# Kernel optimization log

Measured on AMD Instinct MI355X. Metric: run time of the kernel, lower is better.

Reference implementation:

```python
import jax, jax.numpy as jnp
import numpy as np
from math import isqrt

NUM_HEADS = 8
EPS = 1e-12  # torch F.normalize default eps


def _l2_normalize_seq(t):
    # normalize over the sequence axis (dim=-2), matching F.normalize(t, dim=-2)
    n = jnp.sqrt(jnp.sum(t * t, axis=-2, keepdims=True))
    return t / jnp.maximum(n, EPS)


def setup_inputs() -> dict:
    key = jax.random.key(0)
    ks = jax.random.split(key, 7)
    B, L, C = 8, 4096, 384
    s = 0.02
    return {
        "x": jax.random.normal(ks[0], (B, L, C), jnp.float32),
        "qkv_w": jax.random.normal(ks[1], (3 * C, C), jnp.float32) * s,
        "qkv_b": jax.random.normal(ks[2], (3 * C,), jnp.float32) * s,
        "proj_w": jax.random.normal(ks[3], (C, C), jnp.float32) * s,
        "proj_b": jax.random.normal(ks[4], (C,), jnp.float32) * s,
        "temperature": jnp.ones((NUM_HEADS, 1, 1), jnp.float32),
        "conv_w": jax.random.normal(ks[5], (C, 1, 3, 3), jnp.float32) * s,
        "conv_b": jax.random.normal(ks[6], (C,), jnp.float32) * s,
    }


def reference(x, qkv_w, qkv_b, proj_w, proj_b, temperature, conv_w, conv_b):
    B, L, C = x.shape
    h = NUM_HEADS
    d = C // h
    H = W = isqrt(L)

    # qkv projection -> (3, B, h, L, d)
    qkv = (x @ qkv_w.T + qkv_b).reshape(B, L, 3, h, d).transpose(2, 0, 3, 1, 4)
    q, k, v = qkv[0], qkv[1], qkv[2]

    # L2 normalize q, k over sequence axis
    q = _l2_normalize_seq(q)
    k = _l2_normalize_seq(k)

    # LePE: depthwise 3x3 conv on v in image layout (B, C, H, W)
    v_img = v.transpose(0, 1, 3, 2).reshape(B, C, H, W)
    lepe = jax.lax.conv_general_dilated(
        v_img, conv_w, window_strides=(1, 1), padding=((1, 1), (1, 1)),
        feature_group_count=C,
        dimension_numbers=("NCHW", "OIHW", "NCHW"),
    ) + conv_b[None, :, None, None]
    lepe = lepe.reshape(B, h, d, L).transpose(0, 1, 3, 2)  # (B, h, L, d)

    # linear attention: attn = (k^T v) * temperature, shape (B, h, d, d)
    attn = jnp.einsum("bhld,bhle->bhde", k, v) * temperature
    out = jnp.einsum("bhld,bhde->bhle", q, attn) + lepe  # (B, h, L, d)

    out = out.transpose(0, 2, 1, 3).reshape(B, L, C)
    out = out @ proj_w.T + proj_b
    return (out, attn)
```

## Files before the change

### kernel.cpp

```cpp
#include <hip/hip_runtime.h>
#include <hip/hip_bf16.h>


typedef __bf16 bf16x8 __attribute__((ext_vector_type(8)));
typedef float f32x4 __attribute__((ext_vector_type(4)));

__device__ inline __bf16 f2b(float f) {
    __hip_bfloat16 h = __float2bfloat16(f);
    __bf16 r; __builtin_memcpy(&r, &h, 2); return r;
}
__device__ inline float b2f(__hip_bfloat16 h) { return __bfloat162float(h); }
__device__ inline float b2f(__bf16 v) {
    __hip_bfloat16 h; __builtin_memcpy(&h, &v, 2); return __bfloat162float(h);
}

__device__ inline bf16x8 load8(const __hip_bfloat16* p) {
    uint4 v = *(const uint4*)p;
    bf16x8 r; __builtin_memcpy(&r, &v, 16); return r;
}
__device__ inline bf16x8 load8(const float* p) {
    float4 a = *(const float4*)p;
    float4 b = *(const float4*)(p + 4);
    bf16x8 r;
    r[0] = f2b(a.x); r[1] = f2b(a.y); r[2] = f2b(a.z); r[3] = f2b(a.w);
    r[4] = f2b(b.x); r[5] = f2b(b.y); r[6] = f2b(b.z); r[7] = f2b(b.w);
    return r;
}

__device__ inline void storef(float* p, float v) { *p = v; }
__device__ inline void storef(__hip_bfloat16* p, float v) { *p = __float2bfloat16(v); }

__device__ inline void gl_lds16(const __hip_bfloat16* g, __hip_bfloat16* l) {
    __builtin_amdgcn_global_load_lds(
        (const __attribute__((address_space(1))) void*)g,
        (__attribute__((address_space(3))) void*)l,
        16, 0, 0);
}

__global__ __launch_bounds__(256) void cvt_kernel(
    const float* __restrict__ x,  __hip_bfloat16* __restrict__ xb,
    const float* __restrict__ qw, __hip_bfloat16* __restrict__ qwb,
    const float* __restrict__ pw, __hip_bfloat16* __restrict__ pwb)
{
    int blk = blockIdx.x;
    const float* src; __hip_bfloat16* dst; int base;
    if (blk < 6144)      { src = x;  dst = xb;  base = blk; }
    else if (blk < 6360) { src = qw; dst = qwb; base = blk - 6144; }
    else                 { src = pw; dst = pwb; base = blk - 6360; }
    int i = base * 256 + threadIdx.x;
    bf16x8 v = load8(src + (size_t)i * 8);
    *(bf16x8*)(dst + (size_t)i * 8) = v;
}

template <typename TO, int KC, bool FUSE_SQ>
__global__ __launch_bounds__(256) void gemm_bf16_nt(
    const __hip_bfloat16* __restrict__ A,
    const __hip_bfloat16* __restrict__ Bw,
    const float* __restrict__ bias,
    TO* __restrict__ C,
    int N, int NXT,
    float* __restrict__ sq)
{
    __shared__ __hip_bfloat16 As[128 * 64];
    __shared__ __hip_bfloat16 Bs[64 * 64];
    const int t = threadIdx.x;
    const int w = t >> 6, lane = t & 63;
    const int r16 = lane & 15, quad = lane >> 4;
    const int bx  = blockIdx.x;
    const int xcd = bx & 7, seq = bx >> 3;
    const int n_t = seq % NXT, m_t = seq / NXT;
    const int m0 = (xcd + 8 * m_t) * 128;
    const int n0 = n_t * 64;
    const int wm = w >> 1, wn = w & 1;

    f32x4 acc[4][2];
    #pragma unroll
    for (int mi = 0; mi < 4; ++mi)
        #pragma unroll
        for (int ni = 0; ni < 2; ++ni)
            acc[mi][ni] = (f32x4){0.f, 0.f, 0.f, 0.f};

    for (int k0 = 0; k0 < KC; k0 += 64) {
        #pragma unroll
        for (int p = 0; p < 4; ++p) {
            int c = p * 64 + lane;
            int rl = c >> 3;
            int cc = (c & 7) ^ (rl & 7);
            gl_lds16(A + (size_t)(m0 + w * 32 + rl) * KC + k0 + cc * 8,
                     &As[(w * 256 + c) * 8]);
        }
        #pragma unroll
        for (int p = 0; p < 2; ++p) {
            int c = p * 64 + lane;
            int rl = c >> 3;
            int cc = (c & 7) ^ (rl & 7);
            gl_lds16(Bw + (size_t)(n0 + w * 16 + rl) * KC + k0 + cc * 8,
                     &Bs[(w * 128 + c) * 8]);
        }
        __syncthreads();
        bf16x8 af[4][2], bfr[2][2];
        #pragma unroll
        for (int ks = 0; ks < 2; ++ks) {
            #pragma unroll
            for (int mi = 0; mi < 4; ++mi) {
                int row = wm * 64 + mi * 16 + r16;
                int pc  = (ks * 4 + quad) ^ (r16 & 7);
                af[mi][ks] = *(const bf16x8*)&As[row * 64 + pc * 8];
            }
            #pragma unroll
            for (int ni = 0; ni < 2; ++ni) {
                int row = wn * 32 + ni * 16 + r16;
                int pc  = (ks * 4 + quad) ^ (r16 & 7);
                bfr[ni][ks] = *(const bf16x8*)&Bs[row * 64 + pc * 8];
            }
        }
        #pragma unroll
        for (int ks = 0; ks < 2; ++ks)
            #pragma unroll
            for (int mi = 0; mi < 4; ++mi)
                #pragma unroll
                for (int ni = 0; ni < 2; ++ni)
                    acc[mi][ni] = __builtin_amdgcn_mfma_f32_16x16x32_bf16(
                        af[mi][ks], bfr[ni][ks], acc[mi][ni], 0, 0, 0);
        __syncthreads();
    }

    #pragma unroll
    for (int ni = 0; ni < 2; ++ni) {
        int col = n0 + wn * 32 + ni * 16 + r16;
        float bv = bias[col];
        float s = 0.f;
        #pragma unroll
        for (int mi = 0; mi < 4; ++mi) {
            #pragma unroll
            for (int reg = 0; reg < 4; ++reg) {
                int row = m0 + wm * 64 + mi * 16 + quad * 4 + reg;
                float o = acc[mi][ni][reg] + bv;
                storef(&C[(size_t)row * N + col], o);
                s += o * o;
            }
        }
        if constexpr (FUSE_SQ) {
            if (col < 768) {
                s += __shfl_xor(s, 16);
                s += __shfl_xor(s, 32);
                if (quad == 0) {
                    int b = m0 >> 12;
                    atomicAdd(&sq[b * 768 + col], s);
                }
            }
        }
    }
}

__global__ void invnorm_kernel(const float* __restrict__ sumsq, float* __restrict__ invn)
{
    int i = blockIdx.x * 256 + threadIdx.x;
    if (i < 6144) invn[i] = 1.f / fmaxf(sqrtf(sumsq[i]), 1e-12f);
}

__global__ __launch_bounds__(256) void ktv_mfma_kernel(
    const __hip_bfloat16* __restrict__ qkv, float* __restrict__ G)
{
    __shared__ __hip_bfloat16 kT[4][48][40];
    __shared__ __hip_bfloat16 vT[4][48][40];
    __shared__ float red[4][48][49];

    const int bh = blockIdx.y; const int b = bh >> 3; const int h = bh & 7;
    const int lbase = blockIdx.x * 1024;
    const int t = threadIdx.x;
    const int w = t >> 6, lane = t & 63;
    const int r16 = lane & 15, quad = lane >> 4;

    f32x4 acc[3][3];
    #pragma unroll
    for (int mi = 0; mi < 3; ++mi)
        #pragma unroll
        for (int ni = 0; ni < 3; ++ni)
            acc[mi][ni] = (f32x4){0.f, 0.f, 0.f, 0.f};

    const int mat  = t & 1;
    const int lrow = t >> 1;
    const int tile = lrow >> 5, l_in = lrow & 31;
    const __hip_bfloat16* src = qkv + 384 + mat * 384 + h * 48;
    __hip_bfloat16* dstT = (mat ? &vT[0][0][0] : &kT[0][0][0]) + ((size_t)tile * 48 * 40 + l_in);

    for (int it = 0; it < 8; ++it) {
        const int l0 = lbase + it * 128;
        const __hip_bfloat16* p = src + (size_t)(b * 4096 + l0 + lrow) * 1152;
        __hip_bfloat16 row[48];
        #pragma unroll
        for (int j = 0; j < 6; ++j) {
            uint4 v = *(const uint4*)(p + j * 8);
            __builtin_memcpy(&row[j * 8], &v, 16);
        }
        #pragma unroll
        for (int d = 0; d < 48; ++d)
            dstT[d * 40] = row[d];
        __syncthreads();

        bf16x8 af[3], bfr[3];
        #pragma unroll
        for (int mi = 0; mi < 3; ++mi)
            af[mi] = *(const bf16x8*)&kT[w][mi * 16 + r16][quad * 8];
        #pragma unroll
        for (int ni = 0; ni < 3; ++ni)
            bfr[ni] = *(const bf16x8*)&vT[w][ni * 16 + r16][quad * 8];
        #pragma unroll
        for (int mi = 0; mi < 3; ++mi)
            #pragma unroll
            for (int ni = 0; ni < 3; ++ni)
                acc[mi][ni] = __builtin_amdgcn_mfma_f32_16x16x32_bf16(af[mi], bfr[ni], acc[mi][ni], 0, 0, 0);
        __syncthreads();
    }

    #pragma unroll
    for (int mi = 0; mi < 3; ++mi)
        #pragma unroll
        for (int ni = 0; ni < 3; ++ni)
            #pragma unroll
            for (int reg = 0; reg < 4; ++reg)
                red[w][mi * 16 + quad * 4 + reg][ni * 16 + r16] = acc[mi][ni][reg];
    __syncthreads();

    float* Gb = G + (size_t)bh * 2304;
    for (int cell = t; cell < 2304; cell += 256) {
        int row = cell / 48, col = cell % 48;
        float s = red[0][row][col] + red[1][row][col] + red[2][row][col] + red[3][row][col];
        atomicAdd(&Gb[cell], s);
    }
}

__global__ void scale_attn_kernel(
    const float* __restrict__ G, const float* __restrict__ invn,
    const float* __restrict__ temp,
    float* __restrict__ attn_out, float* __restrict__ attn2)
{
    int bh = blockIdx.x; int b = bh >> 3; int h = bh & 7;
    float tf = temp[h];
    int t = threadIdx.x;
    for (int e = t; e < 2304; e += 256) {
        int dk = e / 48;
        float ink = invn[b * 768 + 384 + h * 48 + dk];
        float inq = invn[b * 768 + h * 48 + dk];
        float av  = G[(size_t)bh * 2304 + e] * ink * tf;
        attn_out[(size_t)bh * 2304 + e] = av;
        attn2[(size_t)bh * 2304 + e]    = av * inq;
    }
}

__global__ __launch_bounds__(256) void qattn_lepe_mfma(
    const __hip_bfloat16* __restrict__ qkv, const float* __restrict__ attn2,
    const float* __restrict__ conv_w, const float* __restrict__ conv_b,
    __hip_bfloat16* __restrict__ y)
{
    __shared__ __attribute__((aligned(16))) char smem[26624];
    __hip_bfloat16 (*qs)[72]  = (__hip_bfloat16 (*)[72])smem;
    __hip_bfloat16 (*a2s)[72] = (__hip_bfloat16 (*)[72])(smem + 18432);
    float (*ys)[52]           = (float (*)[52])smem;
    __shared__ __hip_bfloat16 vs[4][64][48];
    __shared__ float cwT[9][48];
    __shared__ float cb[48];

    const int bh = blockIdx.y; const int b = bh >> 3; const int h = bh & 7;
    const int yi0 = blockIdx.x * 2;
    const int l0  = yi0 * 64;
    const int t = threadIdx.x;
    const int w = t >> 6, lane = t & 63;
    const int r16 = lane & 15, quad = lane >> 4;

    const __hip_bfloat16* qbase = qkv + (size_t)(b * 4096 + l0) * 1152 + h * 48;
    #pragma unroll
    for (int i = 0; i < 3; ++i) {
        int chunk = t + i * 256;
        int row = chunk / 6, cg = chunk % 6;
        *(bf16x8*)&qs[row][cg * 8] = load8(qbase + (size_t)row * 1152 + cg * 8);
    }
    *(bf16x8*)&qs[t >> 1][48 + (t & 1) * 8] = (bf16x8)0;

    const float* a2g = attn2 + (size_t)bh * 2304;
    for (int i = t; i < 3072; i += 256) {
        int e = i >> 6, dd = i & 63;
        float val = (dd < 48) ? a2g[dd * 48 + e] : 0.f;
        a2s[e][dd] = __float2bfloat16(val);
    }

    const __hip_bfloat16* vbase = qkv + (size_t)b * 4096 * 1152 + 768 + h * 48;
    #pragma unroll
    for (int i = 0; i < 6; ++i) {
        int chunk = t + i * 256;
        int r = chunk / 384, rem = chunk % 384;
        int xx = rem / 6, cg = rem % 6;
        int yy = yi0 - 1 + r;
        bf16x8 v = (yy >= 0 && yy < 64)
            ? load8(vbase + (size_t)(yy * 64 + xx) * 1152 + cg * 8)
            : (bf16x8)0;
        *(bf16x8*)&vs[r][xx][cg * 8] = v;
    }

    for (int i = t; i < 432; i += 256)
        cwT[i / 48][i % 48] = conv_w[(h * 48 + (i % 48)) * 9 + (i / 48)];
    if (t < 48) cb[t] = conv_b[h * 48 + t];
    __syncthreads();

    f32x4 acc[2][3];
    #pragma unroll
    for (int mi = 0; mi < 2; ++mi)
        #pragma unroll
        for (int ni = 0; ni < 3; ++ni)
            acc[mi][ni] = (f32x4){0.f, 0.f, 0.f, 0.f};
    #pragma unroll
    for (int ks = 0; ks < 2; ++ks) {
        int kb = ks * 32 + quad * 8;
        bf16x8 af[2], bfr[3];
        #pragma unroll
        for (int mi = 0; mi < 2; ++mi)
            af[mi] = *(const bf16x8*)&qs[w * 32 + mi * 16 + r16][kb];
        #pragma unroll
        for (int ni = 0; ni < 3; ++ni)
            bfr[ni] = *(const bf16x8*)&a2s[ni * 16 + r16][kb];
        #pragma unroll
        for (int mi = 0; mi < 2; ++mi)
            #pragma unroll
            for (int ni = 0; ni < 3; ++ni)
                acc[mi][ni] = __builtin_amdgcn_mfma_f32_16x16x32_bf16(af[mi], bfr[ni], acc[mi][ni], 0, 0, 0);
    }
    __syncthreads();

    #pragma unroll
    for (int mi = 0; mi < 2; ++mi)
        #pragma unroll
        for (int ni = 0; ni < 3; ++ni)
            #pragma unroll
            for (int reg = 0; reg < 4; ++reg)
                ys[w * 32 + mi * 16 + quad * 4 + reg][ni * 16 + r16] = acc[mi][ni][reg];
    __syncthreads();

    __hip_bfloat16* ybase = y + (size_t)(b * 4096 + l0) * 384 + h * 48;
    #pragma unroll
    for (int i = 0; i < 3; ++i) {
        int g = t + i * 256;
        int l_in = g / 6, cg = g % 6, e0 = cg * 8;
        int xi = l_in & 63, vr0 = l_in >> 6;
        float o[8];
        #pragma unroll
        for (int j = 0; j < 8; ++j) o[j] = ys[l_in][e0 + j] + cb[e0 + j];
        #pragma unroll
        for (int dy = 0; dy < 3; ++dy) {
            #pragma unroll
            for (int dx = 0; dx < 3; ++dx) {
                int xx = xi + dx - 1;
                if (xx < 0 || xx > 63) continue;
                bf16x8 vv = *(const bf16x8*)&vs[vr0 + dy][xx][e0];
                const float* cwp = &cwT[dy * 3 + dx][e0];
                #pragma unroll
                for (int j = 0; j < 8; ++j) o[j] += b2f(vv[j]) * cwp[j];
            }
        }
        __hip_bfloat16 ob[8];
        #pragma unroll
        for (int j = 0; j < 8; ++j) ob[j] = __float2bfloat16(o[j]);
        uint4 pk; __builtin_memcpy(&pk, ob, 16);
        *(uint4*)(ybase + (size_t)l_in * 384 + e0) = pk;
    }
}

extern "C" void kernel_launch(void* const* d_in, const int* in_sizes, int n_in,
                              void* d_out, int out_size, void* d_ws, size_t ws_size,
                              hipStream_t stream)
{
    const float* x      = (const float*)d_in[0];
    const float* qkv_w  = (const float*)d_in[1];
    const float* qkv_b  = (const float*)d_in[2];
    const float* proj_w = (const float*)d_in[3];
    const float* proj_b = (const float*)d_in[4];
    const float* temp   = (const float*)d_in[5];
    const float* conv_w = (const float*)d_in[6];
    const float* conv_b = (const float*)d_in[7];

    char* ws = (char*)d_ws;
    __hip_bfloat16* qkv = (__hip_bfloat16*)(ws);
    __hip_bfloat16* yb  = (__hip_bfloat16*)(ws + 75497472);
    float* sumsq = (float*)(ws + 100663296);
    float* G     = (float*)(ws + 100687872);
    float* invn  = (float*)(ws + 101277696);
    float* attn2 = (float*)(ws + 101302272);
    __hip_bfloat16* x_bf16  = yb;
    __hip_bfloat16* qkv_wb  = (__hip_bfloat16*)(ws + 101892096);
    __hip_bfloat16* proj_wb = (__hip_bfloat16*)(ws + 102776832);

    float* out      = (float*)d_out;
    float* attn_out = out + 12582912;

    (void)hipMemsetAsync(ws + 100663296, 0, 614400, stream);

    cvt_kernel<<<6432, 256, 0, stream>>>(x, x_bf16, qkv_w, qkv_wb, proj_w, proj_wb);
    gemm_bf16_nt<__hip_bfloat16, 384, true><<<4608, 256, 0, stream>>>(
        x_bf16, qkv_wb, qkv_b, qkv, 1152, 18, sumsq);
    invnorm_kernel<<<24, 256, 0, stream>>>(sumsq, invn);
    ktv_mfma_kernel<<<dim3(4, 64), 256, 0, stream>>>(qkv, G);
    scale_attn_kernel<<<64, 256, 0, stream>>>(G, invn, temp, attn_out, attn2);
    qattn_lepe_mfma<<<dim3(32, 64), 256, 0, stream>>>(qkv, attn2, conv_w, conv_b, yb);
    gemm_bf16_nt<float, 384, false><<<1536, 256, 0, stream>>>(
        yb, proj_wb, proj_b, out, 384, 6, nullptr);
}
```

Before: 226.1 us.

## Fuse x fp32-to-bf16 conversion into QKV GEMM and drop invnorm kernel

The QKV GEMM now reads fp32 x directly and converts it to bf16 in registers before storing to LDS, so the separate conversion pass that wrote and re-read a bf16 copy of x goes away. The inverse-norm computation moves into scale_attn_kernel through shared memory, which removes one launch. The k^T v kernel is split across 4x more blocks (256 rows each instead of 1024) to raise occupancy, at the cost of more atomic adds into G. The A-tile load in the QKV GEMM loses its asynchronous global-to-LDS path and now takes twice the bytes through registers.

```diff
diff --git a/kernel.cpp b/kernel.cpp
--- a/kernel.cpp
+++ b/kernel.cpp
@@ -38,23 +38,21 @@
 }
 
 __global__ __launch_bounds__(256) void cvt_kernel(
-    const float* __restrict__ x,  __hip_bfloat16* __restrict__ xb,
     const float* __restrict__ qw, __hip_bfloat16* __restrict__ qwb,
     const float* __restrict__ pw, __hip_bfloat16* __restrict__ pwb)
 {
     int blk = blockIdx.x;
     const float* src; __hip_bfloat16* dst; int base;
-    if (blk < 6144)      { src = x;  dst = xb;  base = blk; }
-    else if (blk < 6360) { src = qw; dst = qwb; base = blk - 6144; }
-    else                 { src = pw; dst = pwb; base = blk - 6360; }
+    if (blk < 216) { src = qw; dst = qwb; base = blk; }
+    else           { src = pw; dst = pwb; base = blk - 216; }
     int i = base * 256 + threadIdx.x;
     bf16x8 v = load8(src + (size_t)i * 8);
     *(bf16x8*)(dst + (size_t)i * 8) = v;
 }
 
-template <typename TO, int KC, bool FUSE_SQ>
+template <typename TA, typename TO, int KC, bool FUSE_SQ>
 __global__ __launch_bounds__(256) void gemm_bf16_nt(
-    const __hip_bfloat16* __restrict__ A,
+    const TA* __restrict__ A,
     const __hip_bfloat16* __restrict__ Bw,
     const float* __restrict__ bias,
     TO* __restrict__ C,
@@ -82,20 +80,36 @@
 
     for (int k0 = 0; k0 < KC; k0 += 64) {
         #pragma unroll
-        for (int p = 0; p < 4; ++p) {
-            int c = p * 64 + lane;
-            int rl = c >> 3;
-            int cc = (c & 7) ^ (rl & 7);
-            gl_lds16(A + (size_t)(m0 + w * 32 + rl) * KC + k0 + cc * 8,
-                     &As[(w * 256 + c) * 8]);
-        }
-        #pragma unroll
         for (int p = 0; p < 2; ++p) {
             int c = p * 64 + lane;
             int rl = c >> 3;
             int cc = (c & 7) ^ (rl & 7);
             gl_lds16(Bw + (size_t)(n0 + w * 16 + rl) * KC + k0 + cc * 8,
                      &Bs[(w * 128 + c) * 8]);
+        }
+        if constexpr (__is_same(TA, float)) {
+            #pragma unroll
+            for (int p = 0; p < 4; ++p) {
+                int c = p * 64 + lane;
+                int rl = c >> 3;
+                int cc = (c & 7) ^ (rl & 7);
+                const float* src = A + (size_t)(m0 + w * 32 + rl) * KC + k0 + cc * 8;
+                float4 a = *(const float4*)src;
+                float4 b = *(const float4*)(src + 4);
+                bf16x8 r;
+                r[0] = f2b(a.x); r[1] = f2b(a.y); r[2] = f2b(a.z); r[3] = f2b(a.w);
+                r[4] = f2b(b.x); r[5] = f2b(b.y); r[6] = f2b(b.z); r[7] = f2b(b.w);
+                *(bf16x8*)&As[(w * 256 + c) * 8] = r;
+            }
+        } else {
+            #pragma unroll
+            for (int p = 0; p < 4; ++p) {
+                int c = p * 64 + lane;
+                int rl = c >> 3;
+                int cc = (c & 7) ^ (rl & 7);
+                gl_lds16(A + (size_t)(m0 + w * 32 + rl) * KC + k0 + cc * 8,
+                         &As[(w * 256 + c) * 8]);
+            }
         }
         __syncthreads();
         bf16x8 af[4][2], bfr[2][2];
@@ -153,12 +167,6 @@
     }
 }
 
-__global__ void invnorm_kernel(const float* __restrict__ sumsq, float* __restrict__ invn)
-{
-    int i = blockIdx.x * 256 + threadIdx.x;
-    if (i < 6144) invn[i] = 1.f / fmaxf(sqrtf(sumsq[i]), 1e-12f);
-}
-
 __global__ __launch_bounds__(256) void ktv_mfma_kernel(
     const __hip_bfloat16* __restrict__ qkv, float* __restrict__ G)
 {
@@ -167,7 +175,7 @@
     __shared__ float red[4][48][49];
 
     const int bh = blockIdx.y; const int b = bh >> 3; const int h = bh & 7;
-    const int lbase = blockIdx.x * 1024;
+    const int lbase = blockIdx.x * 256;
     const int t = threadIdx.x;
     const int w = t >> 6, lane = t & 63;
     const int r16 = lane & 15, quad = lane >> 4;
@@ -185,7 +193,7 @@
     const __hip_bfloat16* src = qkv + 384 + mat * 384 + h * 48;
     __hip_bfloat16* dstT = (mat ? &vT[0][0][0] : &kT[0][0][0]) + ((size_t)tile * 48 * 40 + l_in);
 
-    for (int it = 0; it < 8; ++it) {
+    for (int it = 0; it < 2; ++it) {
         const int l0 = lbase + it * 128;
         const __hip_bfloat16* p = src + (size_t)(b * 4096 + l0 + lrow) * 1152;
         __hip_bfloat16 row[48];
@@ -232,20 +240,24 @@
 }
 
 __global__ void scale_attn_kernel(
-    const float* __restrict__ G, const float* __restrict__ invn,
+    const float* __restrict__ G, const float* __restrict__ sumsq,
     const float* __restrict__ temp,
     float* __restrict__ attn_out, float* __restrict__ attn2)
 {
     int bh = blockIdx.x; int b = bh >> 3; int h = bh & 7;
     float tf = temp[h];
     int t = threadIdx.x;
+    __shared__ float ink_s[48], inq_s[48];
+    if (t < 48) {
+        ink_s[t] = 1.f / fmaxf(sqrtf(sumsq[b * 768 + 384 + h * 48 + t]), 1e-12f);
+        inq_s[t] = 1.f / fmaxf(sqrtf(sumsq[b * 768 +       h * 48 + t]), 1e-12f);
+    }
+    __syncthreads();
     for (int e = t; e < 2304; e += 256) {
         int dk = e / 48;
-        float ink = invn[b * 768 + 384 + h * 48 + dk];
-        float inq = invn[b * 768 + h * 48 + dk];
-        float av  = G[(size_t)bh * 2304 + e] * ink * tf;
+        float av  = G[(size_t)bh * 2304 + e] * ink_s[dk] * tf;
         attn_out[(size_t)bh * 2304 + e] = av;
-        attn2[(size_t)bh * 2304 + e]    = av * inq;
+        attn2[(size_t)bh * 2304 + e]    = av * inq_s[dk];
     }
 }
 
@@ -383,9 +395,7 @@
     __hip_bfloat16* yb  = (__hip_bfloat16*)(ws + 75497472);
     float* sumsq = (float*)(ws + 100663296);
     float* G     = (float*)(ws + 100687872);
-    float* invn  = (float*)(ws + 101277696);
     float* attn2 = (float*)(ws + 101302272);
-    __hip_bfloat16* x_bf16  = yb;
     __hip_bfloat16* qkv_wb  = (__hip_bfloat16*)(ws + 101892096);
     __hip_bfloat16* proj_wb = (__hip_bfloat16*)(ws + 102776832);
 
@@ -394,13 +404,12 @@
 
     (void)hipMemsetAsync(ws + 100663296, 0, 614400, stream);
 
-    cvt_kernel<<<6432, 256, 0, stream>>>(x, x_bf16, qkv_w, qkv_wb, proj_w, proj_wb);
-    gemm_bf16_nt<__hip_bfloat16, 384, true><<<4608, 256, 0, stream>>>(
-        x_bf16, qkv_wb, qkv_b, qkv, 1152, 18, sumsq);
-    invnorm_kernel<<<24, 256, 0, stream>>>(sumsq, invn);
-    ktv_mfma_kernel<<<dim3(4, 64), 256, 0, stream>>>(qkv, G);
-    scale_attn_kernel<<<64, 256, 0, stream>>>(G, invn, temp, attn_out, attn2);
+    cvt_kernel<<<288, 256, 0, stream>>>(qkv_w, qkv_wb, proj_w, proj_wb);
+    gemm_bf16_nt<float, __hip_bfloat16, 384, true><<<4608, 256, 0, stream>>>(
+        x, qkv_wb, qkv_b, qkv, 1152, 18, sumsq);
+    ktv_mfma_kernel<<<dim3(16, 64), 256, 0, stream>>>(qkv, G);
+    scale_attn_kernel<<<64, 256, 0, stream>>>(G, sumsq, temp, attn_out, attn2);
     qattn_lepe_mfma<<<dim3(32, 64), 256, 0, stream>>>(qkv, attn2, conv_w, conv_b, yb);
-    gemm_bf16_nt<float, 384, false><<<1536, 256, 0, stream>>>(
+    gemm_bf16_nt<__hip_bfloat16, float, 384, false><<<1536, 256, 0, stream>>>(
         yb, proj_wb, proj_b, out, 384, 6, nullptr);
 }
```

Result: slower. 245.4 us (+8.5%).

## Double-buffer GEMM LDS tiles, fold invnorm into scale kernel, widen k^T v grid

Applied to the files above, without the earlier changes.

The bf16 GEMM now uses two LDS buffers and issues the next K-tile's global-to-LDS loads before the MFMA work on the current tile, to overlap memory with compute. The separate inverse-norm kernel is removed; scale_attn computes the inverse norms itself into shared memory, saving a launch. The k^T v kernel uses four times more blocks, each covering fewer rows, for more parallelism at the cost of more atomic adds. LDS use in the GEMM doubles, which may reduce occupancy.

```diff
diff --git a/kernel.cpp b/kernel.cpp
--- a/kernel.cpp
+++ b/kernel.cpp
@@ -61,8 +61,8 @@
     int N, int NXT,
     float* __restrict__ sq)
 {
-    __shared__ __hip_bfloat16 As[128 * 64];
-    __shared__ __hip_bfloat16 Bs[64 * 64];
+    __shared__ __hip_bfloat16 As[2][128 * 64];
+    __shared__ __hip_bfloat16 Bs[2][64 * 64];
     const int t = threadIdx.x;
     const int w = t >> 6, lane = t & 63;
     const int r16 = lane & 15, quad = lane >> 4;
@@ -80,14 +80,14 @@
         for (int ni = 0; ni < 2; ++ni)
             acc[mi][ni] = (f32x4){0.f, 0.f, 0.f, 0.f};
 
-    for (int k0 = 0; k0 < KC; k0 += 64) {
+    auto stage = [&](int buf, int k0) {
         #pragma unroll
         for (int p = 0; p < 4; ++p) {
             int c = p * 64 + lane;
             int rl = c >> 3;
             int cc = (c & 7) ^ (rl & 7);
             gl_lds16(A + (size_t)(m0 + w * 32 + rl) * KC + k0 + cc * 8,
-                     &As[(w * 256 + c) * 8]);
+                     &As[buf][(w * 256 + c) * 8]);
         }
         #pragma unroll
         for (int p = 0; p < 2; ++p) {
@@ -95,9 +95,17 @@
             int rl = c >> 3;
             int cc = (c & 7) ^ (rl & 7);
             gl_lds16(Bw + (size_t)(n0 + w * 16 + rl) * KC + k0 + cc * 8,
-                     &Bs[(w * 128 + c) * 8]);
-        }
-        __syncthreads();
+                     &Bs[buf][(w * 128 + c) * 8]);
+        }
+    };
+
+    constexpr int NT = KC / 64;
+    stage(0, 0);
+    __syncthreads();
+
+    #pragma unroll
+    for (int ti = 0; ti < NT; ++ti) {
+        const int cur = ti & 1;
         bf16x8 af[4][2], bfr[2][2];
         #pragma unroll
         for (int ks = 0; ks < 2; ++ks) {
@@ -105,15 +113,16 @@
             for (int mi = 0; mi < 4; ++mi) {
                 int row = wm * 64 + mi * 16 + r16;
                 int pc  = (ks * 4 + quad) ^ (r16 & 7);
-                af[mi][ks] = *(const bf16x8*)&As[row * 64 + pc * 8];
+                af[mi][ks] = *(const bf16x8*)&As[cur][row * 64 + pc * 8];
             }
             #pragma unroll
             for (int ni = 0; ni < 2; ++ni) {
                 int row = wn * 32 + ni * 16 + r16;
                 int pc  = (ks * 4 + quad) ^ (r16 & 7);
-                bfr[ni][ks] = *(const bf16x8*)&Bs[row * 64 + pc * 8];
+                bfr[ni][ks] = *(const bf16x8*)&Bs[cur][row * 64 + pc * 8];
             }
         }
+        if (ti + 1 < NT) stage(cur ^ 1, (ti + 1) * 64);
         #pragma unroll
         for (int ks = 0; ks < 2; ++ks)
             #pragma unroll
@@ -153,12 +162,6 @@
     }
 }
 
-__global__ void invnorm_kernel(const float* __restrict__ sumsq, float* __restrict__ invn)
-{
-    int i = blockIdx.x * 256 + threadIdx.x;
-    if (i < 6144) invn[i] = 1.f / fmaxf(sqrtf(sumsq[i]), 1e-12f);
-}
-
 __global__ __launch_bounds__(256) void ktv_mfma_kernel(
     const __hip_bfloat16* __restrict__ qkv, float* __restrict__ G)
 {
@@ -167,7 +170,7 @@
     __shared__ float red[4][48][49];
 
     const int bh = blockIdx.y; const int b = bh >> 3; const int h = bh & 7;
-    const int lbase = blockIdx.x * 1024;
+    const int lbase = blockIdx.x * 256;
     const int t = threadIdx.x;
     const int w = t >> 6, lane = t & 63;
     const int r16 = lane & 15, quad = lane >> 4;
@@ -185,7 +188,7 @@
     const __hip_bfloat16* src = qkv + 384 + mat * 384 + h * 48;
     __hip_bfloat16* dstT = (mat ? &vT[0][0][0] : &kT[0][0][0]) + ((size_t)tile * 48 * 40 + l_in);
 
-    for (int it = 0; it < 8; ++it) {
+    for (int it = 0; it < 2; ++it) {
         const int l0 = lbase + it * 128;
         const __hip_bfloat16* p = src + (size_t)(b * 4096 + l0 + lrow) * 1152;
         __hip_bfloat16 row[48];
@@ -232,20 +235,24 @@
 }
 
 __global__ void scale_attn_kernel(
-    const float* __restrict__ G, const float* __restrict__ invn,
+    const float* __restrict__ G, const float* __restrict__ sumsq,
     const float* __restrict__ temp,
     float* __restrict__ attn_out, float* __restrict__ attn2)
 {
     int bh = blockIdx.x; int b = bh >> 3; int h = bh & 7;
     float tf = temp[h];
     int t = threadIdx.x;
+    __shared__ float ink_s[48], inq_s[48];
+    if (t < 48) {
+        ink_s[t] = 1.f / fmaxf(sqrtf(sumsq[b * 768 + 384 + h * 48 + t]), 1e-12f);
+        inq_s[t] = 1.f / fmaxf(sqrtf(sumsq[b * 768 +       h * 48 + t]), 1e-12f);
+    }
+    __syncthreads();
     for (int e = t; e < 2304; e += 256) {
         int dk = e / 48;
-        float ink = invn[b * 768 + 384 + h * 48 + dk];
-        float inq = invn[b * 768 + h * 48 + dk];
-        float av  = G[(size_t)bh * 2304 + e] * ink * tf;
+        float av  = G[(size_t)bh * 2304 + e] * ink_s[dk] * tf;
         attn_out[(size_t)bh * 2304 + e] = av;
-        attn2[(size_t)bh * 2304 + e]    = av * inq;
+        attn2[(size_t)bh * 2304 + e]    = av * inq_s[dk];
     }
 }
 
@@ -383,7 +390,6 @@
     __hip_bfloat16* yb  = (__hip_bfloat16*)(ws + 75497472);
     float* sumsq = (float*)(ws + 100663296);
     float* G     = (float*)(ws + 100687872);
-    float* invn  = (float*)(ws + 101277696);
     float* attn2 = (float*)(ws + 101302272);
     __hip_bfloat16* x_bf16  = yb;
     __hip_bfloat16* qkv_wb  = (__hip_bfloat16*)(ws + 101892096);
@@ -397,9 +403,8 @@
     cvt_kernel<<<6432, 256, 0, stream>>>(x, x_bf16, qkv_w, qkv_wb, proj_w, proj_wb);
     gemm_bf16_nt<__hip_bfloat16, 384, true><<<4608, 256, 0, stream>>>(
         x_bf16, qkv_wb, qkv_b, qkv, 1152, 18, sumsq);
-    invnorm_kernel<<<24, 256, 0, stream>>>(sumsq, invn);
-    ktv_mfma_kernel<<<dim3(4, 64), 256, 0, stream>>>(qkv, G);
-    scale_attn_kernel<<<64, 256, 0, stream>>>(G, invn, temp, attn_out, attn2);
+    ktv_mfma_kernel<<<dim3(16, 64), 256, 0, stream>>>(qkv, G);
+    scale_attn_kernel<<<64, 256, 0, stream>>>(G, sumsq, temp, attn_out, attn2);
     qattn_lepe_mfma<<<dim3(32, 64), 256, 0, stream>>>(qkv, attn2, conv_w, conv_b, yb);
     gemm_bf16_nt<float, 384, false><<<1536, 256, 0, stream>>>(
         yb, proj_wb, proj_b, out, 384, 6, nullptr);
```

Measured after the change: 222.8 us. Within noise of the previous version (-1.5%).

## Fold norm and attn scaling into qattn kernel, zero accumulators in cvt, widen ktv grid

Applied to the files above, without the earlier changes.

Removes the invnorm and scale_attn kernels and the memset. The inverse norms and temperature scaling are now computed inside qattn_lepe_mfma from sumsq and the raw G, and block x==0 writes attn_out. Zeroing of the accumulators moves into extra blocks of cvt_kernel. ktv is split into 16 blocks per head instead of 4 to raise parallelism, at the cost of more atomic adds on G and redundant per-block norm computation.

```diff
diff --git a/kernel.cpp b/kernel.cpp
--- a/kernel.cpp
+++ b/kernel.cpp
@@ -40,9 +40,14 @@
 __global__ __launch_bounds__(256) void cvt_kernel(
     const float* __restrict__ x,  __hip_bfloat16* __restrict__ xb,
     const float* __restrict__ qw, __hip_bfloat16* __restrict__ qwb,
-    const float* __restrict__ pw, __hip_bfloat16* __restrict__ pwb)
+    const float* __restrict__ pw, __hip_bfloat16* __restrict__ pwb,
+    uint4* __restrict__ zdst)
 {
     int blk = blockIdx.x;
+    if (blk >= 6432) {
+        zdst[(size_t)(blk - 6432) * 256 + threadIdx.x] = (uint4){0, 0, 0, 0};
+        return;
+    }
     const float* src; __hip_bfloat16* dst; int base;
     if (blk < 6144)      { src = x;  dst = xb;  base = blk; }
     else if (blk < 6360) { src = qw; dst = qwb; base = blk - 6144; }
@@ -153,12 +158,6 @@
     }
 }
 
-__global__ void invnorm_kernel(const float* __restrict__ sumsq, float* __restrict__ invn)
-{
-    int i = blockIdx.x * 256 + threadIdx.x;
-    if (i < 6144) invn[i] = 1.f / fmaxf(sqrtf(sumsq[i]), 1e-12f);
-}
-
 __global__ __launch_bounds__(256) void ktv_mfma_kernel(
     const __hip_bfloat16* __restrict__ qkv, float* __restrict__ G)
 {
@@ -167,7 +166,7 @@
     __shared__ float red[4][48][49];
 
     const int bh = blockIdx.y; const int b = bh >> 3; const int h = bh & 7;
-    const int lbase = blockIdx.x * 1024;
+    const int lbase = blockIdx.x * 256;
     const int t = threadIdx.x;
     const int w = t >> 6, lane = t & 63;
     const int r16 = lane & 15, quad = lane >> 4;
@@ -185,7 +184,7 @@
     const __hip_bfloat16* src = qkv + 384 + mat * 384 + h * 48;
     __hip_bfloat16* dstT = (mat ? &vT[0][0][0] : &kT[0][0][0]) + ((size_t)tile * 48 * 40 + l_in);
 
-    for (int it = 0; it < 8; ++it) {
+    for (int it = 0; it < 2; ++it) {
         const int l0 = lbase + it * 128;
         const __hip_bfloat16* p = src + (size_t)(b * 4096 + l0 + lrow) * 1152;
         __hip_bfloat16 row[48];
@@ -231,28 +230,11 @@
     }
 }
 
-__global__ void scale_attn_kernel(
-    const float* __restrict__ G, const float* __restrict__ invn,
-    const float* __restrict__ temp,
-    float* __restrict__ attn_out, float* __restrict__ attn2)
-{
-    int bh = blockIdx.x; int b = bh >> 3; int h = bh & 7;
-    float tf = temp[h];
-    int t = threadIdx.x;
-    for (int e = t; e < 2304; e += 256) {
-        int dk = e / 48;
-        float ink = invn[b * 768 + 384 + h * 48 + dk];
-        float inq = invn[b * 768 + h * 48 + dk];
-        float av  = G[(size_t)bh * 2304 + e] * ink * tf;
-        attn_out[(size_t)bh * 2304 + e] = av;
-        attn2[(size_t)bh * 2304 + e]    = av * inq;
-    }
-}
-
 __global__ __launch_bounds__(256) void qattn_lepe_mfma(
-    const __hip_bfloat16* __restrict__ qkv, const float* __restrict__ attn2,
+    const __hip_bfloat16* __restrict__ qkv, const float* __restrict__ G,
+    const float* __restrict__ sumsq, const float* __restrict__ temp,
     const float* __restrict__ conv_w, const float* __restrict__ conv_b,
-    __hip_bfloat16* __restrict__ y)
+    __hip_bfloat16* __restrict__ y, float* __restrict__ attn_out)
 {
     __shared__ __attribute__((aligned(16))) char smem[26624];
     __hip_bfloat16 (*qs)[72]  = (__hip_bfloat16 (*)[72])smem;
@@ -261,6 +243,7 @@
     __shared__ __hip_bfloat16 vs[4][64][48];
     __shared__ float cwT[9][48];
     __shared__ float cb[48];
+    __shared__ float ink_s[48], inq_s[48];
 
     const int bh = blockIdx.y; const int b = bh >> 3; const int h = bh & 7;
     const int yi0 = blockIdx.x * 2;
@@ -268,6 +251,20 @@
     const int t = threadIdx.x;
     const int w = t >> 6, lane = t & 63;
     const int r16 = lane & 15, quad = lane >> 4;
+    const float tf = temp[h];
+
+    if (t < 48) {
+        ink_s[t] = 1.f / fmaxf(sqrtf(sumsq[b * 768 + 384 + h * 48 + t]), 1e-12f);
+        inq_s[t] = 1.f / fmaxf(sqrtf(sumsq[b * 768 +       h * 48 + t]), 1e-12f);
+    }
+    __syncthreads();
+
+    const float* Gb = G + (size_t)bh * 2304;
+
+    if (blockIdx.x == 0) {
+        for (int e = t; e < 2304; e += 256)
+            attn_out[(size_t)bh * 2304 + e] = Gb[e] * ink_s[e / 48] * tf;
+    }
 
     const __hip_bfloat16* qbase = qkv + (size_t)(b * 4096 + l0) * 1152 + h * 48;
     #pragma unroll
@@ -278,10 +275,13 @@
     }
     *(bf16x8*)&qs[t >> 1][48 + (t & 1) * 8] = (bf16x8)0;
 
-    const float* a2g = attn2 + (size_t)bh * 2304;
     for (int i = t; i < 3072; i += 256) {
         int e = i >> 6, dd = i & 63;
-        float val = (dd < 48) ? a2g[dd * 48 + e] : 0.f;
+        float val = 0.f;
+        if (dd < 48) {
+            float av = Gb[dd * 48 + e] * ink_s[dd] * tf;
+            val = av * inq_s[dd];
+        }
         a2s[e][dd] = __float2bfloat16(val);
     }
 
@@ -383,8 +383,6 @@
     __hip_bfloat16* yb  = (__hip_bfloat16*)(ws + 75497472);
     float* sumsq = (float*)(ws + 100663296);
     float* G     = (float*)(ws + 100687872);
-    float* invn  = (float*)(ws + 101277696);
-    float* attn2 = (float*)(ws + 101302272);
     __hip_bfloat16* x_bf16  = yb;
     __hip_bfloat16* qkv_wb  = (__hip_bfloat16*)(ws + 101892096);
     __hip_bfloat16* proj_wb = (__hip_bfloat16*)(ws + 102776832);
@@ -392,15 +390,13 @@
     float* out      = (float*)d_out;
     float* attn_out = out + 12582912;
 
-    (void)hipMemsetAsync(ws + 100663296, 0, 614400, stream);
-
-    cvt_kernel<<<6432, 256, 0, stream>>>(x, x_bf16, qkv_w, qkv_wb, proj_w, proj_wb);
+    cvt_kernel<<<6582, 256, 0, stream>>>(x, x_bf16, qkv_w, qkv_wb, proj_w, proj_wb,
+                                         (uint4*)(ws + 100663296));
     gemm_bf16_nt<__hip_bfloat16, 384, true><<<4608, 256, 0, stream>>>(
         x_bf16, qkv_wb, qkv_b, qkv, 1152, 18, sumsq);
-    invnorm_kernel<<<24, 256, 0, stream>>>(sumsq, invn);
-    ktv_mfma_kernel<<<dim3(4, 64), 256, 0, stream>>>(qkv, G);
-    scale_attn_kernel<<<64, 256, 0, stream>>>(G, invn, temp, attn_out, attn2);
-    qattn_lepe_mfma<<<dim3(32, 64), 256, 0, stream>>>(qkv, attn2, conv_w, conv_b, yb);
+    ktv_mfma_kernel<<<dim3(16, 64), 256, 0, stream>>>(qkv, G);
+    qattn_lepe_mfma<<<dim3(32, 64), 256, 0, stream>>>(
+        qkv, G, sumsq, temp, conv_w, conv_b, yb, attn_out);
     gemm_bf16_nt<float, 384, false><<<1536, 256, 0, stream>>>(
         yb, proj_wb, proj_b, out, 384, 6, nullptr);
 }
```

New measurement: 219.3 us. 3.0% less time.
